# Performance work log

Measured on AMD Instinct MI355X. Metric: run time of the kernel, lower is better.

Reference implementation:

```python
import jax, jax.numpy as jnp
import numpy as np

EPS = 1e-5

def _layernorm(x, g, b):
    mu = jnp.mean(x, axis=-1, keepdims=True)
    var = jnp.mean(jnp.square(x - mu), axis=-1, keepdims=True)
    return (x - mu) * jax.lax.rsqrt(var + EPS) * g + b

def setup_inputs() -> dict:
    key = jax.random.key(0)
    ks = jax.random.split(key, 8)
    B, T, D, H = 2, 2048, 1024, 16
    hd = D // H
    s = 0.02
    return {
        "x": jax.random.normal(ks[0], (B, T, D), jnp.float32),
        "wq": jax.random.normal(ks[1], (H, D, hd), jnp.float32) * s,
        "wk": jax.random.normal(ks[2], (H, D, hd), jnp.float32) * s,
        "wv": jax.random.normal(ks[3], (H, D, hd), jnp.float32) * s,
        "w_proj": jax.random.normal(ks[4], (D, D), jnp.float32) * s,
        "b_proj": jnp.zeros((D,), jnp.float32),
        "w_ff1": jax.random.normal(ks[5], (D, 4 * D), jnp.float32) * s,
        "b_ff1": jnp.zeros((4 * D,), jnp.float32),
        "w_ff2": jax.random.normal(ks[6], (4 * D, D), jnp.float32) * s,
        "b_ff2": jnp.zeros((D,), jnp.float32),
        "ln1_g": jnp.ones((D,), jnp.float32),
        "ln1_b": jnp.zeros((D,), jnp.float32),
        "ln2_g": jnp.ones((D,), jnp.float32),
        "ln2_b": jnp.zeros((D,), jnp.float32),
    }

def reference(x, wq, wk, wv, w_proj, b_proj, w_ff1, b_ff1, w_ff2, b_ff2,
              ln1_g, ln1_b, ln2_g, ln2_b):
    B, T, D = x.shape
    H, _, hd = wq.shape
    # --- self-attention sublayer (pre-LN) ---
    h = _layernorm(x, ln1_g, ln1_b)
    # per-head Q/K/V projections batched over heads (math identical to per-head linears)
    q = jnp.einsum('btd,hds->bhts', h, wq)
    k = jnp.einsum('btd,hds->bhts', h, wk)
    v = jnp.einsum('btd,hds->bhts', h, wv)
    att = jnp.einsum('bhts,bhTs->bhtT', q, k) * (hd ** -0.5)  # [B,H,T,T]
    causal = jnp.tril(jnp.ones((T, T), dtype=bool))
    att = jnp.where(causal, att, jnp.float32(-jnp.inf))
    att = jax.nn.softmax(att, axis=-1)
    o = jnp.einsum('bhtT,bhTs->bhts', att, v)                 # [B,H,T,hd]
    o = o.transpose(0, 2, 1, 3).reshape(B, T, H * hd)         # concat heads
    x = x + o @ w_proj + b_proj
    # --- FFN sublayer (pre-LN) ---
    h2 = _layernorm(x, ln2_g, ln2_b)
    ff = jax.nn.relu(h2 @ w_ff1 + b_ff1) @ w_ff2 + b_ff2
    return x + ff
```

## Files before the change

### kernel.cpp

```cpp
#include <hip/hip_runtime.h>

typedef unsigned short u16;
typedef unsigned int   u32;
typedef __bf16 bf16;
typedef bf16 bf16x8 __attribute__((ext_vector_type(8)));
typedef float f32x4 __attribute__((ext_vector_type(4)));
typedef u32 u32x4 __attribute__((ext_vector_type(4)));

__device__ inline u16 f2bf(float f) {
  union { float f; u32 u; } cv; cv.f = f;
  u32 u = cv.u;
  return (u16)((u + 0x7FFFu + ((u >> 16) & 1u)) >> 16);
}

__device__ __forceinline__ void gld16(const void* g, void* l) {
  __builtin_amdgcn_global_load_lds(
      (const __attribute__((address_space(1))) void*)g,
      (__attribute__((address_space(3))) void*)l, 16, 0, 0);
}

__global__ __launch_bounds__(256) void ln_kernel(
    const float* __restrict__ x, const float* __restrict__ g,
    const float* __restrict__ b, u16* __restrict__ out)
{
  const int row = blockIdx.x;
  const int t = threadIdx.x;
  const float4 v = *reinterpret_cast<const float4*>(&x[(size_t)row*1024 + t*4]);
  float s  = v.x + v.y + v.z + v.w;
  float sq = v.x*v.x + v.y*v.y + v.z*v.z + v.w*v.w;
  #pragma unroll
  for (int off = 32; off; off >>= 1) { s += __shfl_down(s, off); sq += __shfl_down(sq, off); }
  __shared__ float red[8];
  const int wave = t >> 6, lane = t & 63;
  if (lane == 0) { red[wave] = s; red[wave + 4] = sq; }
  __syncthreads();
  __shared__ float stats[2];
  if (t == 0) {
    float S  = red[0] + red[1] + red[2] + red[3];
    float SQ = red[4] + red[5] + red[6] + red[7];
    float mu = S * (1.0f/1024.0f);
    float var = SQ * (1.0f/1024.0f) - mu*mu;
    stats[0] = mu; stats[1] = rsqrtf(var + 1e-5f);
  }
  __syncthreads();
  const float mu = stats[0], rv = stats[1];
  const float4 gv = *reinterpret_cast<const float4*>(&g[t*4]);
  const float4 bv = *reinterpret_cast<const float4*>(&b[t*4]);
  u16 o4[4];
  o4[0] = f2bf((v.x - mu)*rv*gv.x + bv.x);
  o4[1] = f2bf((v.y - mu)*rv*gv.y + bv.y);
  o4[2] = f2bf((v.z - mu)*rv*gv.z + bv.z);
  o4[3] = f2bf((v.w - mu)*rv*gv.w + bv.w);
  u32 p0 = (u32)o4[0] | ((u32)o4[1] << 16);
  u32 p1 = (u32)o4[2] | ((u32)o4[3] << 16);
  u32* op = reinterpret_cast<u32*>(&out[(size_t)row*1024 + t*4]);
  op[0] = p0; op[1] = p1;
}

__global__ __launch_bounds__(256) void transpose_cast(
    const float* __restrict__ in, u16* __restrict__ out, int R, int C)
{
  __shared__ float tile[32][33];
  const int tx = threadIdx.x, ty = threadIdx.y;
  const size_t bo = (size_t)blockIdx.z * R * C;
  const int r0 = blockIdx.y * 32, c0 = blockIdx.x * 32;
  #pragma unroll
  for (int j = 0; j < 4; ++j)
    tile[ty + j*8][tx] = in[bo + (size_t)(r0 + ty + j*8)*C + c0 + tx];
  __syncthreads();
  #pragma unroll
  for (int j = 0; j < 4; ++j)
    out[bo + (size_t)(c0 + ty + j*8)*R + r0 + tx] = f2bf(tile[tx][ty + j*8]);
}

__global__ __launch_bounds__(256) void vt_kernel(
    const u16* __restrict__ qkv, u16* __restrict__ vt, int T)
{
  __shared__ u16 tile[32][33];
  const int tx = threadIdx.x, ty = threadIdx.y;
  const int bh = blockIdx.z, b = bh >> 4, h = bh & 15;
  const int r0 = blockIdx.x * 32;
  const int c0 = blockIdx.y * 32;
  const size_t tokbase = (size_t)b * T;
  #pragma unroll
  for (int j = 0; j < 4; ++j)
    tile[ty + j*8][tx] = qkv[(tokbase + r0 + ty + j*8)*3072 + 2048 + h*64 + c0 + tx];
  __syncthreads();
  #pragma unroll
  for (int j = 0; j < 4; ++j)
    vt[((size_t)bh*64 + c0 + ty + j*8)*T + r0 + tx] = tile[tx][ty + j*8];
}

__global__ __launch_bounds__(512, 2) void gemm_128(
    const u16* __restrict__ A, const u16* __restrict__ BT,
    int M, int N, int K,
    const float* __restrict__ bias, const float* __restrict__ resid,
    float* __restrict__ Cout)
{
  __shared__ __align__(16) u16 Alds[2][128*64];
  __shared__ __align__(16) u16 Blds[2][128*64];
  const int t = threadIdx.x;
  const int wave = t >> 6, lane = t & 63;
  const int wm = wave >> 2, wn = wave & 3;
  const int g = lane >> 4, r = lane & 15;
  const int m0 = blockIdx.y * 128, n0 = blockIdx.x * 128;
  const int NTk = K >> 6;

  f32x4 acc[4][2] = {};

  auto STAGE = [&](int buf, int kt) {
    const int k0 = kt << 6;
    #pragma unroll
    for (int p = 0; p < 2; ++p) {
      const int c = t + p*512;
      const int row = c >> 3;
      const int col = (((c & 7) ^ (row & 7)) << 3);
      gld16(&A[(size_t)(m0 + row)*K + k0 + col], &Alds[buf][c*8]);
    }
    #pragma unroll
    for (int p = 0; p < 2; ++p) {
      const int c = t + p*512;
      const int row = c >> 3;
      const int col = (((c & 7) ^ (row & 7)) << 3);
      gld16(&BT[(size_t)(n0 + row)*K + k0 + col], &Blds[buf][c*8]);
    }
  };

  STAGE(0, 0);
  if (NTk > 1) STAGE(1, 1);

  const int csw = (r & 7) << 3;

  for (int kt = 0; kt < NTk; ++kt) {
    const int buf = kt & 1;
    if (kt + 1 < NTk) asm volatile("s_waitcnt vmcnt(4)" ::: "memory");
    else              asm volatile("s_waitcnt vmcnt(0)" ::: "memory");
    __builtin_amdgcn_s_barrier();
    #pragma unroll
    for (int ks = 0; ks < 2; ++ks) {
      bf16x8 af[4], bfr[2];
      #pragma unroll
      for (int i = 0; i < 4; ++i)
        af[i] = *reinterpret_cast<const bf16x8*>(
            &Alds[buf][(wm*64 + i*16 + r)*64 + ((ks*32 + g*8) ^ csw)]);
      #pragma unroll
      for (int j = 0; j < 2; ++j)
        bfr[j] = *reinterpret_cast<const bf16x8*>(
            &Blds[buf][(wn*32 + j*16 + r)*64 + ((ks*32 + g*8) ^ csw)]);
      __builtin_amdgcn_s_setprio(1);
      #pragma unroll
      for (int i = 0; i < 4; ++i)
        #pragma unroll
        for (int j = 0; j < 2; ++j)
          acc[i][j] = __builtin_amdgcn_mfma_f32_16x16x32_bf16(af[i], bfr[j], acc[i][j], 0, 0, 0);
      __builtin_amdgcn_s_setprio(0);
      __builtin_amdgcn_s_barrier();
    }
    if (kt + 2 < NTk) STAGE(buf, kt + 2);
  }

  #pragma unroll
  for (int mi = 0; mi < 4; ++mi) {
    #pragma unroll
    for (int ni = 0; ni < 2; ++ni) {
      #pragma unroll
      for (int i = 0; i < 4; ++i) {
        const int gm = m0 + wm*64 + mi*16 + g*4 + i;
        const int gn = n0 + wn*32 + ni*16 + r;
        const size_t idx = (size_t)gm * N + gn;
        Cout[idx] = acc[mi][ni][i] + bias[gn] + resid[idx];
      }
    }
  }
}

template<int EPI>
__global__ __launch_bounds__(512, 2) void gemm_bt8(
    const u16* __restrict__ A, const u16* __restrict__ BT,
    int M, int N, int K,
    const float* __restrict__ bias, void* __restrict__ Cout)
{
  __shared__ __align__(16) u16 Alds[2][256*64];
  __shared__ __align__(16) u16 Blds[2][256*64];
  const int t = threadIdx.x;
  const int wave = t >> 6, lane = t & 63;
  const int wm = wave >> 2, wn = wave & 3;
  const int g = lane >> 4, r = lane & 15;
  const int m0 = blockIdx.y * 256, n0 = blockIdx.x * 256;
  const int NTk = K >> 6;

  f32x4 acc[8][4] = {};

  auto STAGE = [&](int buf, int kt) {
    const int k0 = kt << 6;
    #pragma unroll
    for (int p = 0; p < 4; ++p) {
      const int c = t + p*512;
      const int row = c >> 3;
      const int col = (((c & 7) ^ (row & 7)) << 3);
      gld16(&A[(size_t)(m0 + row)*K + k0 + col], &Alds[buf][c*8]);
    }
    #pragma unroll
    for (int p = 0; p < 4; ++p) {
      const int c = t + p*512;
      const int row = c >> 3;
      const int col = (((c & 7) ^ (row & 7)) << 3);
      gld16(&BT[(size_t)(n0 + row)*K + k0 + col], &Blds[buf][c*8]);
    }
  };

  STAGE(0, 0);
  if (NTk > 1) STAGE(1, 1);

  const int csw = (r & 7) << 3;

  for (int kt = 0; kt < NTk; ++kt) {
    const int buf = kt & 1;
    if (kt + 1 < NTk) asm volatile("s_waitcnt vmcnt(8)" ::: "memory");
    else              asm volatile("s_waitcnt vmcnt(0)" ::: "memory");
    __builtin_amdgcn_s_barrier();
    #pragma unroll
    for (int p = 0; p < 4; ++p) {
      const int ks = p >> 1, mih = p & 1;
      bf16x8 af[4], bfr[4];
      #pragma unroll
      for (int i = 0; i < 4; ++i) {
        af[i] = *reinterpret_cast<const bf16x8*>(
            &Alds[buf][(wm*128 + (mih*4 + i)*16 + r)*64 + ((ks*32 + g*8) ^ csw)]);
        bfr[i] = *reinterpret_cast<const bf16x8*>(
            &Blds[buf][(wn*64 + i*16 + r)*64 + ((ks*32 + g*8) ^ csw)]);
      }
      __builtin_amdgcn_s_setprio(1);
      #pragma unroll
      for (int i = 0; i < 4; ++i)
        #pragma unroll
        for (int j = 0; j < 4; ++j)
          acc[mih*4 + i][j] =
              __builtin_amdgcn_mfma_f32_16x16x32_bf16(af[i], bfr[j], acc[mih*4 + i][j], 0, 0, 0);
      __builtin_amdgcn_s_setprio(0);
      __builtin_amdgcn_s_barrier();
    }
    if (kt + 2 < NTk) STAGE(buf, kt + 2);
  }

  #pragma unroll
  for (int mi = 0; mi < 8; ++mi) {
    #pragma unroll
    for (int ni = 0; ni < 4; ++ni) {
      #pragma unroll
      for (int i = 0; i < 4; ++i) {
        const int gm = m0 + wm*128 + mi*16 + g*4 + i;
        const int gn = n0 + wn*64 + ni*16 + r;
        const size_t idx = (size_t)gm * N + gn;
        float v = acc[mi][ni][i];
        if (EPI == 0) {
          const float sc = (gn < 1024) ? 0.18033688011112042f : 1.0f;
          ((u16*)Cout)[idx] = f2bf(v * sc);
        } else {
          v += bias[gn];
          ((u16*)Cout)[idx] = f2bf(v > 0.f ? v : 0.f);
        }
      }
    }
  }
}

__global__ __launch_bounds__(256, 4) void attn_kernel(
    const u16* __restrict__ qkv, const u16* __restrict__ vt,
    u16* __restrict__ o, int T)
{
  const int bid = blockIdx.x;
  const int swz = (bid & 7) * 128 + (bid >> 3);
  const int idx = swz & 31;
  const int qa  = (idx & 1) ? ((idx - 1) >> 1) : (31 - (idx >> 1));
  const int bh  = swz >> 5;
  const int b = bh >> 4, h = bh & 15;
  const int t = threadIdx.x;
  const int wave = t >> 6, lane = t & 63;
  const int g = lane >> 4, r = lane & 15;
  const size_t tokbase = (size_t)b * T;
  const int q0 = qa*64 + wave*16;

  __shared__ __align__(16) u16 Klds[2][64*64];
  __shared__ __align__(16) u16 Vlds[2][64*64];
  __shared__ __align__(16) u16 P[4][16*64];

  bf16x8 qf[2];
  #pragma unroll
  for (int ks = 0; ks < 2; ++ks)
    qf[ks] = *reinterpret_cast<const bf16x8*>(
        &qkv[(tokbase + q0 + r)*3072 + h*64 + ks*32 + g*8]);

  bf16x8 ones;
  #pragma unroll
  for (int i = 0; i < 8; ++i) ones[i] = (bf16)1.0f;

  f32x4 acc_o[4] = {};
  f32x4 acc_l = {};

  const int nkv = qa + 1;

  auto STAGE = [&](int buf, int kb) {
    const int kv0 = kb*64;
    #pragma unroll
    for (int p = 0; p < 2; ++p) {
      const int c2 = t + p*256;
      const int row = c2 >> 3;
      const int scol = ((c2 & 7) ^ (row & 7)) << 3;
      gld16(&qkv[(tokbase + kv0 + row)*3072 + 1024 + h*64 + scol], &Klds[buf][c2*8]);
      gld16(&vt[((size_t)bh*64 + row)*T + kv0 + scol], &Vlds[buf][c2*8]);
    }
  };

  STAGE(0, 0);
  int cur = 0;
  for (int kb = 0; kb < nkv; ++kb) {
    __syncthreads();
    if (kb + 1 < nkv) STAGE(cur ^ 1, kb + 1);
    const int kv0 = kb*64;
    const bool diag = (kb == qa);
    const int cb = (r & 7) << 3;

    f32x4 s[4] = {};
    #pragma unroll
    for (int nb = 0; nb < 4; ++nb) {
      #pragma unroll
      for (int ks = 0; ks < 2; ++ks) {
        bf16x8 kf = *reinterpret_cast<const bf16x8*>(
            &Klds[cur][(nb*16 + r)*64 + ((ks*32 + g*8) ^ cb)]);
        s[nb] = __builtin_amdgcn_mfma_f32_16x16x32_bf16(qf[ks], kf, s[nb], 0, 0, 0);
      }
    }
    #pragma unroll
    for (int i = 0; i < 4; ++i) {
      const int prow = g*4 + i;
      const int pcb = (prow & 7) << 3;
      #pragma unroll
      for (int nb = 0; nb < 4; ++nb) {
        float pv = __builtin_amdgcn_exp2f(s[nb][i]);
        if (diag && (kv0 + nb*16 + r > q0 + prow)) pv = 0.f;
        P[wave][prow*64 + ((nb*16 + r) ^ pcb)] = f2bf(pv);
      }
    }
    #pragma unroll
    for (int ks = 0; ks < 2; ++ks) {
      bf16x8 pf = *reinterpret_cast<const bf16x8*>(
          &P[wave][r*64 + ((ks*32 + g*8) ^ cb)]);
      acc_l = __builtin_amdgcn_mfma_f32_16x16x32_bf16(pf, ones, acc_l, 0, 0, 0);
      #pragma unroll
      for (int nt = 0; nt < 4; ++nt) {
        bf16x8 vf = *reinterpret_cast<const bf16x8*>(
            &Vlds[cur][(nt*16 + r)*64 + ((ks*32 + g*8) ^ cb)]);
        acc_o[nt] = __builtin_amdgcn_mfma_f32_16x16x32_bf16(pf, vf, acc_o[nt], 0, 0, 0);
      }
    }
    cur ^= 1;
  }
  #pragma unroll
  for (int i = 0; i < 4; ++i) {
    const float inv = 1.0f / acc_l[i];
    const size_t rowo = (tokbase + q0 + g*4 + i) * 1024;
    #pragma unroll
    for (int nt = 0; nt < 4; ++nt)
      o[rowo + h*64 + nt*16 + r] = f2bf(acc_o[nt][i] * inv);
  }
}

extern "C" void kernel_launch(void* const* d_in, const int* in_sizes, int n_in,
                              void* d_out, int out_size, void* d_ws, size_t ws_size,
                              hipStream_t stream)
{
  const float* x      = (const float*)d_in[0];
  const float* wq     = (const float*)d_in[1];
  const float* wk     = (const float*)d_in[2];
  const float* wv     = (const float*)d_in[3];
  const float* w_proj = (const float*)d_in[4];
  const float* b_proj = (const float*)d_in[5];
  const float* w_ff1  = (const float*)d_in[6];
  const float* b_ff1  = (const float*)d_in[7];
  const float* w_ff2  = (const float*)d_in[8];
  const float* b_ff2  = (const float*)d_in[9];
  const float* ln1_g  = (const float*)d_in[10];
  const float* ln1_b  = (const float*)d_in[11];
  const float* ln2_g  = (const float*)d_in[12];
  const float* ln2_b  = (const float*)d_in[13];

  const int T = 2048;
  const int NT = 4096;

  char* ws = (char*)d_ws;
  u16* Wbuf   = (u16*)(ws);
  u16* hbuf   = (u16*)(ws + ((size_t)8  << 20));
  u16* qkvbuf = (u16*)(ws + ((size_t)16 << 20));
  u16* obuf   = (u16*)(ws + ((size_t)40 << 20));
  u16* ff1buf = qkvbuf;
  u16* vtbuf  = Wbuf;
  float* x1   = (float*)d_out;

  ln_kernel<<<dim3(NT), dim3(256), 0, stream>>>(x, ln1_g, ln1_b, hbuf);
  transpose_cast<<<dim3(2, 32, 16), dim3(32, 8), 0, stream>>>(wq, Wbuf + 0*1024*1024, 1024, 64);
  transpose_cast<<<dim3(2, 32, 16), dim3(32, 8), 0, stream>>>(wk, Wbuf + 1*1024*1024, 1024, 64);
  transpose_cast<<<dim3(2, 32, 16), dim3(32, 8), 0, stream>>>(wv, Wbuf + 2*1024*1024, 1024, 64);
  gemm_bt8<0><<<dim3(12, 16), dim3(512), 0, stream>>>(hbuf, Wbuf, NT, 3072, 1024, nullptr, qkvbuf);
  vt_kernel<<<dim3(64, 2, 32), dim3(32, 8), 0, stream>>>(qkvbuf, vtbuf, T);
  attn_kernel<<<dim3(1024), dim3(256), 0, stream>>>(qkvbuf, vtbuf, obuf, T);
  transpose_cast<<<dim3(32, 32, 1), dim3(32, 8), 0, stream>>>(w_proj, Wbuf, 1024, 1024);
  gemm_128<<<dim3(8, 32), dim3(512), 0, stream>>>(obuf, Wbuf, NT, 1024, 1024, b_proj, x, x1);
  ln_kernel<<<dim3(NT), dim3(256), 0, stream>>>(x1, ln2_g, ln2_b, hbuf);
  transpose_cast<<<dim3(128, 32, 1), dim3(32, 8), 0, stream>>>(w_ff1, Wbuf, 1024, 4096);
  gemm_bt8<2><<<dim3(16, 16), dim3(512), 0, stream>>>(hbuf, Wbuf, NT, 4096, 1024, b_ff1, ff1buf);
  transpose_cast<<<dim3(32, 128, 1), dim3(32, 8), 0, stream>>>(w_ff2, Wbuf, 4096, 1024);
  gemm_128<<<dim3(8, 32), dim3(512), 0, stream>>>(ff1buf, Wbuf, NT, 1024, 4096, b_ff2, x1, (float*)d_out);
}
```

Before: 267.9 us.

## Split-K atomic GEMMs with residual prefill, paired attention q-blocks per CTA

The residual projection and FFN2 GEMMs become a split-K-by-2 kernel with 256x128 tiles. Each K half accumulates into the output with atomic adds. The residual plus bias is prefilled by the layernorm kernels, which now also write x+bias into the output buffer. The attention kernel now processes a long and a short causal q-block per CTA (512 CTAs) to balance work, and bf16 conversion uses the native cast. This is meant to fix wave quantization and load imbalance, at the cost of atomic traffic, non-deterministic summation, and a change in rounding mode.

```diff
diff --git a/kernel.cpp b/kernel.cpp
--- a/kernel.cpp
+++ b/kernel.cpp
@@ -19,9 +19,11 @@
       (__attribute__((address_space(3))) void*)l, 16, 0, 0);
 }
 
+template<bool ADDB>
 __global__ __launch_bounds__(256) void ln_kernel(
     const float* __restrict__ x, const float* __restrict__ g,
-    const float* __restrict__ b, u16* __restrict__ out)
+    const float* __restrict__ b, u16* __restrict__ out,
+    const float* __restrict__ badd, float* __restrict__ xwb)
 {
   const int row = blockIdx.x;
   const int t = threadIdx.x;
@@ -55,6 +57,12 @@
   u32 p1 = (u32)o4[2] | ((u32)o4[3] << 16);
   u32* op = reinterpret_cast<u32*>(&out[(size_t)row*1024 + t*4]);
   op[0] = p0; op[1] = p1;
+  if (ADDB) {
+    const float4 av = *reinterpret_cast<const float4*>(&badd[t*4]);
+    float4 w;
+    w.x = v.x + av.x; w.y = v.y + av.y; w.z = v.z + av.z; w.w = v.w + av.w;
+    *reinterpret_cast<float4*>(&xwb[(size_t)row*1024 + t*4]) = w;
+  }
 }
 
 __global__ __launch_bounds__(256) void transpose_cast(
@@ -91,27 +99,33 @@
     vt[((size_t)bh*64 + c0 + ty + j*8)*T + r0 + tx] = tile[tx][ty + j*8];
 }
 
-__global__ __launch_bounds__(512, 2) void gemm_128(
+__global__ __launch_bounds__(512, 2) void gemm_sk2(
     const u16* __restrict__ A, const u16* __restrict__ BT,
-    int M, int N, int K,
-    const float* __restrict__ bias, const float* __restrict__ resid,
-    float* __restrict__ Cout)
-{
-  __shared__ __align__(16) u16 Alds[2][128*64];
+    int M, int N, int K, float* __restrict__ Cout)
+{
+  __shared__ __align__(16) u16 Alds[2][256*64];
   __shared__ __align__(16) u16 Blds[2][128*64];
+  const int bid = blockIdx.x;
+  const int xcd = bid & 7;
+  const int j   = bid >> 3;
+  const int Nn  = N >> 7;
+  const int mi_ = ((j & 1) << 3) | xcd;
+  const int ni_ = (j >> 1) & (Nn - 1);
+  const int kh  = j >> (1 + __builtin_ctz(Nn));
+  const int m0 = mi_ * 256, n0 = ni_ * 128;
+  const int kbase = kh * (K >> 1);
   const int t = threadIdx.x;
   const int wave = t >> 6, lane = t & 63;
-  const int wm = wave >> 2, wn = wave & 3;
+  const int wm = wave >> 1, wn = wave & 1;
   const int g = lane >> 4, r = lane & 15;
-  const int m0 = blockIdx.y * 128, n0 = blockIdx.x * 128;
-  const int NTk = K >> 6;
-
-  f32x4 acc[4][2] = {};
+  const int NTk = K >> 7;
+
+  f32x4 acc[4][4] = {};
 
   auto STAGE = [&](int buf, int kt) {
-    const int k0 = kt << 6;
-    #pragma unroll
-    for (int p = 0; p < 2; ++p) {
+    const int k0 = kbase + (kt << 6);
+    #pragma unroll
+    for (int p = 0; p < 4; ++p) {
       const int c = t + p*512;
       const int row = c >> 3;
       const int col = (((c & 7) ^ (row & 7)) << 3);
@@ -133,26 +147,28 @@
 
   for (int kt = 0; kt < NTk; ++kt) {
     const int buf = kt & 1;
-    if (kt + 1 < NTk) asm volatile("s_waitcnt vmcnt(4)" ::: "memory");
+    if (kt + 1 < NTk) asm volatile("s_waitcnt vmcnt(6)" ::: "memory");
     else              asm volatile("s_waitcnt vmcnt(0)" ::: "memory");
     __builtin_amdgcn_s_barrier();
     #pragma unroll
-    for (int ks = 0; ks < 2; ++ks) {
-      bf16x8 af[4], bfr[2];
-      #pragma unroll
-      for (int i = 0; i < 4; ++i)
+    for (int p = 0; p < 4; ++p) {
+      const int ks = p >> 1, mh = p & 1;
+      bf16x8 af[2], bfr[4];
+      #pragma unroll
+      for (int i = 0; i < 2; ++i)
         af[i] = *reinterpret_cast<const bf16x8*>(
-            &Alds[buf][(wm*64 + i*16 + r)*64 + ((ks*32 + g*8) ^ csw)]);
-      #pragma unroll
-      for (int j = 0; j < 2; ++j)
-        bfr[j] = *reinterpret_cast<const bf16x8*>(
-            &Blds[buf][(wn*32 + j*16 + r)*64 + ((ks*32 + g*8) ^ csw)]);
+            &Alds[buf][(wm*64 + (mh*2 + i)*16 + r)*64 + ((ks*32 + g*8) ^ csw)]);
+      #pragma unroll
+      for (int jj = 0; jj < 4; ++jj)
+        bfr[jj] = *reinterpret_cast<const bf16x8*>(
+            &Blds[buf][(wn*64 + jj*16 + r)*64 + ((ks*32 + g*8) ^ csw)]);
       __builtin_amdgcn_s_setprio(1);
       #pragma unroll
-      for (int i = 0; i < 4; ++i)
+      for (int i = 0; i < 2; ++i)
         #pragma unroll
-        for (int j = 0; j < 2; ++j)
-          acc[i][j] = __builtin_amdgcn_mfma_f32_16x16x32_bf16(af[i], bfr[j], acc[i][j], 0, 0, 0);
+        for (int jj = 0; jj < 4; ++jj)
+          acc[mh*2 + i][jj] =
+              __builtin_amdgcn_mfma_f32_16x16x32_bf16(af[i], bfr[jj], acc[mh*2 + i][jj], 0, 0, 0);
       __builtin_amdgcn_s_setprio(0);
       __builtin_amdgcn_s_barrier();
     }
@@ -162,13 +178,12 @@
   #pragma unroll
   for (int mi = 0; mi < 4; ++mi) {
     #pragma unroll
-    for (int ni = 0; ni < 2; ++ni) {
+    for (int ni = 0; ni < 4; ++ni) {
       #pragma unroll
       for (int i = 0; i < 4; ++i) {
         const int gm = m0 + wm*64 + mi*16 + g*4 + i;
-        const int gn = n0 + wn*32 + ni*16 + r;
-        const size_t idx = (size_t)gm * N + gn;
-        Cout[idx] = acc[mi][ni][i] + bias[gn] + resid[idx];
+        const int gn = n0 + wn*64 + ni*16 + r;
+        unsafeAtomicAdd(&Cout[(size_t)gm * N + gn], acc[mi][ni][i]);
       }
     }
   }
@@ -270,35 +285,21 @@
     u16* __restrict__ o, int T)
 {
   const int bid = blockIdx.x;
-  const int swz = (bid & 7) * 128 + (bid >> 3);
-  const int idx = swz & 31;
-  const int qa  = (idx & 1) ? ((idx - 1) >> 1) : (31 - (idx >> 1));
-  const int bh  = swz >> 5;
+  const int bh  = ((bid & 7) << 2) | ((bid >> 3) & 3);
+  const int qb  = bid >> 5;
   const int b = bh >> 4, h = bh & 15;
   const int t = threadIdx.x;
   const int wave = t >> 6, lane = t & 63;
   const int g = lane >> 4, r = lane & 15;
   const size_t tokbase = (size_t)b * T;
-  const int q0 = qa*64 + wave*16;
 
   __shared__ __align__(16) u16 Klds[2][64*64];
   __shared__ __align__(16) u16 Vlds[2][64*64];
   __shared__ __align__(16) u16 P[4][16*64];
 
-  bf16x8 qf[2];
-  #pragma unroll
-  for (int ks = 0; ks < 2; ++ks)
-    qf[ks] = *reinterpret_cast<const bf16x8*>(
-        &qkv[(tokbase + q0 + r)*3072 + h*64 + ks*32 + g*8]);
-
   bf16x8 ones;
   #pragma unroll
   for (int i = 0; i < 8; ++i) ones[i] = (bf16)1.0f;
-
-  f32x4 acc_o[4] = {};
-  f32x4 acc_l = {};
-
-  const int nkv = qa + 1;
 
   auto STAGE = [&](int buf, int kb) {
     const int kv0 = kb*64;
@@ -312,57 +313,77 @@
     }
   };
 
-  STAGE(0, 0);
-  int cur = 0;
-  for (int kb = 0; kb < nkv; ++kb) {
-    __syncthreads();
-    if (kb + 1 < nkv) STAGE(cur ^ 1, kb + 1);
-    const int kv0 = kb*64;
-    const bool diag = (kb == qa);
-    const int cb = (r & 7) << 3;
-
-    f32x4 s[4] = {};
-    #pragma unroll
-    for (int nb = 0; nb < 4; ++nb) {
+  #pragma unroll 1
+  for (int ph = 0; ph < 2; ++ph) {
+    const int qa = ph ? qb : (31 - qb);
+    const int q0 = qa*64 + wave*16;
+    if (ph) __syncthreads();
+
+    bf16x8 qf[2];
+    #pragma unroll
+    for (int ks = 0; ks < 2; ++ks)
+      qf[ks] = *reinterpret_cast<const bf16x8*>(
+          &qkv[(tokbase + q0 + r)*3072 + h*64 + ks*32 + g*8]);
+
+    f32x4 acc_o[4] = {};
+    f32x4 acc_l = {};
+    const int nkv = qa + 1;
+
+    STAGE(0, 0);
+    int cur = 0;
+    for (int kb = 0; kb < nkv; ++kb) {
+      __syncthreads();
+      if (kb + 1 < nkv) STAGE(cur ^ 1, kb + 1);
+      const int kv0 = kb*64;
+      const bool diag = (kb == qa);
+      const int cb = (r & 7) << 3;
+
+      f32x4 s[4] = {};
+      #pragma unroll
+      for (int nb = 0; nb < 4; ++nb) {
+        #pragma unroll
+        for (int ks = 0; ks < 2; ++ks) {
+          bf16x8 kf = *reinterpret_cast<const bf16x8*>(
+              &Klds[cur][(nb*16 + r)*64 + ((ks*32 + g*8) ^ cb)]);
+          s[nb] = __builtin_amdgcn_mfma_f32_16x16x32_bf16(qf[ks], kf, s[nb], 0, 0, 0);
+        }
+      }
+      #pragma unroll
+      for (int i = 0; i < 4; ++i) {
+        const int prow = g*4 + i;
+        const int pcb = (prow & 7) << 3;
+        #pragma unroll
+        for (int nb = 0; nb < 4; ++nb) {
+          float pv = __builtin_amdgcn_exp2f(s[nb][i]);
+          if (diag && (kv0 + nb*16 + r > q0 + prow)) pv = 0.f;
+          const bf16 bv = (bf16)pv;
+          P[wave][prow*64 + ((nb*16 + r) ^ pcb)] = __builtin_bit_cast(u16, bv);
+        }
+      }
       #pragma unroll
       for (int ks = 0; ks < 2; ++ks) {
-        bf16x8 kf = *reinterpret_cast<const bf16x8*>(
-            &Klds[cur][(nb*16 + r)*64 + ((ks*32 + g*8) ^ cb)]);
-        s[nb] = __builtin_amdgcn_mfma_f32_16x16x32_bf16(qf[ks], kf, s[nb], 0, 0, 0);
-      }
+        bf16x8 pf = *reinterpret_cast<const bf16x8*>(
+            &P[wave][r*64 + ((ks*32 + g*8) ^ cb)]);
+        acc_l = __builtin_amdgcn_mfma_f32_16x16x32_bf16(pf, ones, acc_l, 0, 0, 0);
+        #pragma unroll
+        for (int nt = 0; nt < 4; ++nt) {
+          bf16x8 vf = *reinterpret_cast<const bf16x8*>(
+              &Vlds[cur][(nt*16 + r)*64 + ((ks*32 + g*8) ^ cb)]);
+          acc_o[nt] = __builtin_amdgcn_mfma_f32_16x16x32_bf16(pf, vf, acc_o[nt], 0, 0, 0);
+        }
+      }
+      cur ^= 1;
     }
     #pragma unroll
     for (int i = 0; i < 4; ++i) {
-      const int prow = g*4 + i;
-      const int pcb = (prow & 7) << 3;
-      #pragma unroll
-      for (int nb = 0; nb < 4; ++nb) {
-        float pv = __builtin_amdgcn_exp2f(s[nb][i]);
-        if (diag && (kv0 + nb*16 + r > q0 + prow)) pv = 0.f;
-        P[wave][prow*64 + ((nb*16 + r) ^ pcb)] = f2bf(pv);
-      }
-    }
-    #pragma unroll
-    for (int ks = 0; ks < 2; ++ks) {
-      bf16x8 pf = *reinterpret_cast<const bf16x8*>(
-          &P[wave][r*64 + ((ks*32 + g*8) ^ cb)]);
-      acc_l = __builtin_amdgcn_mfma_f32_16x16x32_bf16(pf, ones, acc_l, 0, 0, 0);
+      const float inv = 1.0f / acc_l[i];
+      const size_t rowo = (tokbase + q0 + g*4 + i) * 1024;
       #pragma unroll
       for (int nt = 0; nt < 4; ++nt) {
-        bf16x8 vf = *reinterpret_cast<const bf16x8*>(
-            &Vlds[cur][(nt*16 + r)*64 + ((ks*32 + g*8) ^ cb)]);
-        acc_o[nt] = __builtin_amdgcn_mfma_f32_16x16x32_bf16(pf, vf, acc_o[nt], 0, 0, 0);
-      }
-    }
-    cur ^= 1;
-  }
-  #pragma unroll
-  for (int i = 0; i < 4; ++i) {
-    const float inv = 1.0f / acc_l[i];
-    const size_t rowo = (tokbase + q0 + g*4 + i) * 1024;
-    #pragma unroll
-    for (int nt = 0; nt < 4; ++nt)
-      o[rowo + h*64 + nt*16 + r] = f2bf(acc_o[nt][i] * inv);
+        const bf16 bv = (bf16)(acc_o[nt][i] * inv);
+        o[rowo + h*64 + nt*16 + r] = __builtin_bit_cast(u16, bv);
+      }
+    }
   }
 }
 
@@ -397,18 +418,18 @@
   u16* vtbuf  = Wbuf;
   float* x1   = (float*)d_out;
 
-  ln_kernel<<<dim3(NT), dim3(256), 0, stream>>>(x, ln1_g, ln1_b, hbuf);
+  ln_kernel<true><<<dim3(NT), dim3(256), 0, stream>>>(x, ln1_g, ln1_b, hbuf, b_proj, x1);
   transpose_cast<<<dim3(2, 32, 16), dim3(32, 8), 0, stream>>>(wq, Wbuf + 0*1024*1024, 1024, 64);
   transpose_cast<<<dim3(2, 32, 16), dim3(32, 8), 0, stream>>>(wk, Wbuf + 1*1024*1024, 1024, 64);
   transpose_cast<<<dim3(2, 32, 16), dim3(32, 8), 0, stream>>>(wv, Wbuf + 2*1024*1024, 1024, 64);
   gemm_bt8<0><<<dim3(12, 16), dim3(512), 0, stream>>>(hbuf, Wbuf, NT, 3072, 1024, nullptr, qkvbuf);
   vt_kernel<<<dim3(64, 2, 32), dim3(32, 8), 0, stream>>>(qkvbuf, vtbuf, T);
-  attn_kernel<<<dim3(1024), dim3(256), 0, stream>>>(qkvbuf, vtbuf, obuf, T);
+  attn_kernel<<<dim3(512), dim3(256), 0, stream>>>(qkvbuf, vtbuf, obuf, T);
   transpose_cast<<<dim3(32, 32, 1), dim3(32, 8), 0, stream>>>(w_proj, Wbuf, 1024, 1024);
-  gemm_128<<<dim3(8, 32), dim3(512), 0, stream>>>(obuf, Wbuf, NT, 1024, 1024, b_proj, x, x1);
-  ln_kernel<<<dim3(NT), dim3(256), 0, stream>>>(x1, ln2_g, ln2_b, hbuf);
+  gemm_sk2<<<dim3(256), dim3(512), 0, stream>>>(obuf, Wbuf, NT, 1024, 1024, x1);
+  ln_kernel<true><<<dim3(NT), dim3(256), 0, stream>>>(x1, ln2_g, ln2_b, hbuf, b_ff2, x1);
   transpose_cast<<<dim3(128, 32, 1), dim3(32, 8), 0, stream>>>(w_ff1, Wbuf, 1024, 4096);
   gemm_bt8<2><<<dim3(16, 16), dim3(512), 0, stream>>>(hbuf, Wbuf, NT, 4096, 1024, b_ff1, ff1buf);
   transpose_cast<<<dim3(32, 128, 1), dim3(32, 8), 0, stream>>>(w_ff2, Wbuf, 4096, 1024);
-  gemm_128<<<dim3(8, 32), dim3(512), 0, stream>>>(ff1buf, Wbuf, NT, 1024, 4096, b_ff2, x1, (float*)d_out);
-}
+  gemm_sk2<<<dim3(256), dim3(512), 0, stream>>>(ff1buf, Wbuf, NT, 1024, 4096, (float*)d_out);
+}
```

Result: no change. 272.0 us (+1.5%).
